# Kernel tuning notes

Measured on AMD Instinct MI355X. Metric: run time of the kernel, lower is better.

Reference implementation:

```python
import jax, jax.numpy as jnp
import numpy as np

B, T, D = 2, 2048, 1024
H, HD = 16, 64          # num_heads, head_dim (D == H*HD)
NM, DMIX, DDEC = 5, 32, 64  # 5 mix streams (r,k,v,w,g); LoRA ranks per source thresholds


def setup_inputs() -> dict:
    key = jax.random.key(0)
    ks = jax.random.split(key, 18)
    n = lambda i, shape, s: jax.random.normal(ks[i], shape, dtype=jnp.float32) * s
    return {
        "hidden_states": n(0, (B, T, D), 1.0),
        "time_maa_x": n(1, (1, 1, D), 0.5),
        "time_maa_r": n(2, (1, 1, D), 0.1),
        "time_maa_k": n(3, (1, 1, D), 0.1),
        "time_maa_v": n(4, (1, 1, D), 0.1),
        "time_maa_w": n(5, (1, 1, D), 0.1),
        "time_maa_g": n(6, (1, 1, D), 0.1),
        "time_maa_w1": n(7, (D, NM * DMIX), 0.01),
        "time_maa_w2": n(8, (NM, DMIX, D), 0.01),
        "time_decay": n(9, (1, 1, D), 0.5) - 2.0,  # decay_speed-like, negative mean
        "time_decay_w1": n(10, (D, DDEC), 0.01),
        "time_decay_w2": n(11, (DDEC, D), 0.01),
        "Wq": n(12, (D, D), 0.02),
        "Wk": n(13, (D, D), 0.02),
        "Wv": n(14, (D, D), 0.02),
        "Wo": n(15, (D, D), 0.02),
        "Wg": n(16, (D, D), 0.02),
        "bg": jnp.full((D,), 1.227, dtype=jnp.float32),  # gate bias init from source
    }


def _forward(hidden_states, time_maa_x, time_maa_r, time_maa_k, time_maa_v,
             time_maa_w, time_maa_g, time_maa_w1, time_maa_w2, time_decay,
             time_decay_w1, time_decay_w2, Wq, Wk, Wv, Wo, Wg, bg):
    x = hidden_states
    Bsz, Tlen, d = x.shape
    # token shift: dxprev = x_{t-1} - x_t (zeros at t=0)
    xprev = jnp.pad(x, ((0, 0), (1, 0), (0, 0)))[:, :Tlen]
    dxprev = xprev - x
    # data-dependent LoRA mixing producing 5 per-stream mix coefficients
    xxx = x + dxprev * time_maa_x
    mix = jnp.tanh(xxx @ time_maa_w1).reshape(Bsz, Tlen, NM, DMIX)
    mix = jnp.einsum('btfl,fld->fbtd', mix, time_maa_w2)  # (5, B, T, D)
    mr, mk, mv, mw, mg = mix
    xr = x + dxprev * (time_maa_r + mr)
    xk = x + dxprev * (time_maa_k + mk)
    xv = x + dxprev * (time_maa_v + mv)
    xw = x + dxprev * (time_maa_w + mw)
    xg = x + dxprev * (time_maa_g + mg)
    # projections -> (B, H, T, HD); num_kv_heads == num_heads so repeat_kv is identity
    q = (xr @ Wq).reshape(Bsz, Tlen, H, HD).transpose(0, 2, 1, 3)
    k = (xk @ Wk).reshape(Bsz, Tlen, H, HD).transpose(0, 2, 1, 3)
    v = (xv @ Wv).reshape(Bsz, Tlen, H, HD).transpose(0, 2, 1, 3)
    decay = time_decay + jnp.tanh(xw @ time_decay_w1) @ time_decay_w2
    g_log = -jnp.exp(decay.reshape(Bsz, Tlen, H, HD).transpose(0, 2, 1, 3))  # (B,H,T,HD), <= 0
    gate = jax.nn.silu(xg @ Wg + bg)
    # bonus term from source: k scaled by (1 - exp(g_log))
    k = k * (1.0 - jnp.exp(g_log))
    q = q * (HD ** -0.5)  # fla scale
    # gated linear attention: S_t = diag(exp(g_t)) S_{t-1} + k_t v_t^T ; o_t = q_t @ S_t
    def step(S, qkvg):
        qt, kt, vt, gt = qkvg                       # (B,H,HD) each
        S = S * jnp.exp(gt)[..., None] + kt[..., None] * vt[..., None, :]
        ot = jnp.einsum('bhk,bhkv->bhv', qt, S)
        return S, ot
    S0 = jnp.zeros((Bsz, H, HD, HD), dtype=jnp.float32)
    seq = (jnp.moveaxis(q, 2, 0), jnp.moveaxis(k, 2, 0),
           jnp.moveaxis(v, 2, 0), jnp.moveaxis(g_log, 2, 0))
    _, o = jax.lax.scan(step, S0, seq)              # (T, B, H, HD)
    o = jnp.moveaxis(o, 0, 1)                       # (B, T, H, HD)
    o = o.reshape(Bsz, Tlen, H * HD)
    return (o * gate) @ Wo


def reference(hidden_states, time_maa_x, time_maa_r, time_maa_k, time_maa_v,
              time_maa_w, time_maa_g, time_maa_w1, time_maa_w2, time_decay,
              time_decay_w1, time_decay_w2, Wq, Wk, Wv, Wo, Wg, bg):
    return _forward(hidden_states, time_maa_x, time_maa_r, time_maa_k, time_maa_v,
                    time_maa_w, time_maa_g, time_maa_w1, time_maa_w2, time_decay,
                    time_decay_w1, time_decay_w2, Wq, Wk, Wv, Wo, Wg, bg)
```

## Files before the change

kernel.cpp:

```cpp
#include <hip/hip_runtime.h>
#include <hip/hip_bf16.h>

typedef __hip_bfloat16 bf16;
typedef __bf16 bf16x8 __attribute__((ext_vector_type(8)));
typedef float f32x4 __attribute__((ext_vector_type(4)));

static constexpr size_t MB = 1ull << 20;

static constexpr size_t OFF_XXXQ = 0;
static constexpr size_t OFF_K    = 8  * MB;
static constexpr size_t OFF_V    = 16 * MB;
static constexpr size_t OFF_W    = 24 * MB;
static constexpr size_t OFF_GATE = 32 * MB;
static constexpr size_t OFF_WOT  = 40 * MB;
static constexpr size_t OFF_W1T  = 42 * MB;
static constexpr size_t OFF_WD1T = 42 * MB + 512 * 1024;
static constexpr size_t OFF_WD2T = 42 * MB + 768 * 1024;
static constexpr size_t OFF_MP   = 43 * MB;
static constexpr size_t OFF_DECT = 47 * MB;
static constexpr size_t OFF_XS   = 48 * MB;
static constexpr size_t OFF_WQT  = 56 * MB;
static constexpr size_t OFF_WKT  = 58 * MB;
static constexpr size_t OFF_WVT  = 60 * MB;
static constexpr size_t OFF_WGT  = 62 * MB;
static constexpr size_t OFF_SLOC = 43 * MB;
static constexpr size_t OFF_D    = 59 * MB;

__device__ __forceinline__ void async_ld16(const void* g, void* l) {
    __builtin_amdgcn_global_load_lds((const __attribute__((address_space(1))) void*)g,
                                     (__attribute__((address_space(3))) void*)l, 16, 0, 0);
}
__device__ __forceinline__ float bf2f(unsigned short u) {
    union { unsigned int i; float f; } x; x.i = ((unsigned int)u) << 16; return x.f;
}

__global__ void transpose_all(const float* __restrict__ Wq, const float* __restrict__ Wk,
                              const float* __restrict__ Wv, const float* __restrict__ Wg,
                              const float* __restrict__ Wo, const float* __restrict__ w1,
                              const float* __restrict__ dw1, const float* __restrict__ dw2,
                              bf16* __restrict__ wqt, bf16* __restrict__ wkt,
                              bf16* __restrict__ wvt, bf16* __restrict__ wgt,
                              bf16* __restrict__ wot, bf16* __restrict__ w1t,
                              bf16* __restrict__ wd1t, bf16* __restrict__ wd2t) {
    __shared__ bf16 tile[32][33];
    int id = blockIdx.x;
    const float* src; bf16* dst; int R, C, Cpad, local;
    if      (id < 1024) { src = Wq;  dst = wqt;  R = 1024; C = 1024; Cpad = 1024; local = id; }
    else if (id < 2048) { src = Wk;  dst = wkt;  R = 1024; C = 1024; Cpad = 1024; local = id - 1024; }
    else if (id < 3072) { src = Wv;  dst = wvt;  R = 1024; C = 1024; Cpad = 1024; local = id - 2048; }
    else if (id < 4096) { src = Wg;  dst = wgt;  R = 1024; C = 1024; Cpad = 1024; local = id - 3072; }
    else if (id < 5120) { src = Wo;  dst = wot;  R = 1024; C = 1024; Cpad = 1024; local = id - 4096; }
    else if (id < 5376) { src = w1;  dst = w1t;  R = 1024; C = 160;  Cpad = 256;  local = id - 5120; }
    else if (id < 5504) { src = dw1; dst = wd1t; R = 1024; C = 64;   Cpad = 128;  local = id - 5376; }
    else                { src = dw2; dst = wd2t; R = 64;   C = 1024; Cpad = 1024; local = id - 5504; }
    int Rb = R >> 5;
    int r0 = (local % Rb) * 32, c0 = (local / Rb) * 32;
    int tx = threadIdx.x, ty = threadIdx.y;
#pragma unroll
    for (int yy = 0; yy < 4; ++yy) {
        int r = r0 + ty + yy * 8, c = c0 + tx;
        float v = (r < R && c < C) ? src[(size_t)r * C + c] : 0.f;
        tile[ty + yy * 8][tx] = __float2bfloat16(v);
    }
    __syncthreads();
#pragma unroll
    for (int yy = 0; yy < 4; ++yy) {
        int c = c0 + ty + yy * 8, r = r0 + tx;
        if (c < Cpad && r < R) dst[(size_t)c * R + r] = tile[tx][ty + yy * 8];
    }
}

__global__ void prep_xxx(const float* __restrict__ x, const float* __restrict__ maa_x,
                         bf16* __restrict__ xxx) {
    int i = blockIdx.x * 256 + threadIdx.x;
    int d = i & 1023;
    int t = (i >> 10) & 2047;
    float xv = x[i];
    float xp = (t > 0) ? x[i - 1024] : 0.f;
    xxx[i] = __float2bfloat16(xv + (xp - xv) * maa_x[d]);
}

template<int EPI>
__global__ __launch_bounds__(256)
void gemm_bt(const bf16* __restrict__ A, int lda,
             const bf16* __restrict__ Bt, int ldb,
             void* __restrict__ Cout, int ldc,
             int K, const float* __restrict__ aux)
{
    __shared__ __align__(16) bf16 As[128 * 32];
    __shared__ __align__(16) bf16 Bs[128 * 32];
    const int m0 = blockIdx.x * 128;
    const int n0 = blockIdx.y * 128;
    const int tid = threadIdx.x;
    const int lane = tid & 63;
    const int w = tid >> 6;
    const int wm = w >> 1, wn = w & 1;
    const int row16 = lane & 15;
    const int quad = lane >> 4;

    f32x4 acc[4][4];
#pragma unroll
    for (int mi = 0; mi < 4; ++mi)
#pragma unroll
        for (int ni = 0; ni < 4; ++ni)
            acc[mi][ni] = (f32x4){0.f, 0.f, 0.f, 0.f};

    for (int k0 = 0; k0 < K; k0 += 32) {
        __syncthreads();
#pragma unroll
        for (int j = 0; j < 2; ++j) {
            int i = j * 256 + w * 64 + lane;
            int ri = i >> 2;
            int ci = (i & 3) * 8;
            const bf16* ga = A  + (size_t)(m0 + ri) * lda + (k0 + ci);
            const bf16* gb = Bt + (size_t)(n0 + ri) * ldb + (k0 + ci);
            bf16* la = As + (size_t)(j * 256 + w * 64) * 8;
            bf16* lb = Bs + (size_t)(j * 256 + w * 64) * 8;
            async_ld16(ga, la);
            async_ld16(gb, lb);
        }
        __syncthreads();
        bf16x8 af[4], bfr[4];
#pragma unroll
        for (int mi = 0; mi < 4; ++mi)
            af[mi] = *(const bf16x8*)(As + ((wm * 64 + mi * 16 + row16) * 32 + quad * 8));
#pragma unroll
        for (int ni = 0; ni < 4; ++ni)
            bfr[ni] = *(const bf16x8*)(Bs + ((wn * 64 + ni * 16 + row16) * 32 + quad * 8));
#pragma unroll
        for (int mi = 0; mi < 4; ++mi)
#pragma unroll
            for (int ni = 0; ni < 4; ++ni)
                acc[mi][ni] = __builtin_amdgcn_mfma_f32_16x16x32_bf16(af[mi], bfr[ni], acc[mi][ni], 0, 0, 0);
    }
#pragma unroll
    for (int mi = 0; mi < 4; ++mi)
#pragma unroll
        for (int ni = 0; ni < 4; ++ni)
#pragma unroll
            for (int r = 0; r < 4; ++r) {
                int gr = m0 + wm * 64 + mi * 16 + quad * 4 + r;
                int gc = n0 + wn * 64 + ni * 16 + row16;
                size_t ci = (size_t)gr * ldc + gc;
                float v = acc[mi][ni][r];
                if (EPI == 1) ((float*)Cout)[ci] = tanhf(v);
                else if (EPI == 2) ((bf16*)Cout)[ci] = __float2bfloat16(tanhf(v));
                else if (EPI == 3) {
                    float t = aux[gc] + v;
                    ((bf16*)Cout)[ci] = __float2bfloat16(expf(t));
                } else if (EPI == 4) {
                    float z = v + aux[gc];
                    ((bf16*)Cout)[ci] = __float2bfloat16(z / (1.f + expf(-z)));
                } else if (EPI == 5) {
                    ((bf16*)Cout)[ci] = __float2bfloat16(v);
                } else {
                    ((float*)Cout)[ci] = v;
                }
            }
}

__global__ __launch_bounds__(256)
void mix_stream(const float* __restrict__ mp,
                const float* __restrict__ w2,
                const float* __restrict__ x,
                const float* __restrict__ maa_f,
                int f,
                bf16* __restrict__ xs)
{
    __shared__ float mps[4][32];
    int dg = blockIdx.x;
    int r0 = blockIdx.y * 4;
    int tid = threadIdx.x;
    int d = dg * 256 + tid;
    if (tid < 128) {
        int rr = tid >> 5, l = tid & 31;
        mps[rr][l] = mp[(size_t)(r0 + rr) * 256 + f * 32 + l];
    }
    __syncthreads();
    float acc[4] = {0.f, 0.f, 0.f, 0.f};
#pragma unroll
    for (int l = 0; l < 32; ++l) {
        float wv = w2[(size_t)(f * 32 + l) * 1024 + d];
#pragma unroll
        for (int rr = 0; rr < 4; ++rr)
            acc[rr] = fmaf(mps[rr][l], wv, acc[rr]);
    }
    float mf = maa_f[d];
#pragma unroll
    for (int rr = 0; rr < 4; ++rr) {
        int r = r0 + rr;
        int t = r & 2047;
        size_t i = (size_t)r * 1024 + d;
        float xv = x[i];
        float xp = (t > 0) ? x[i - 1024] : 0.f;
        xs[i] = __float2bfloat16(xv + (xp - xv) * (mf + acc[rr]));
    }
}

__global__ __launch_bounds__(64)
void chunk_state(const bf16* __restrict__ k, const bf16* __restrict__ v,
                 const bf16* __restrict__ w,
                 float* __restrict__ Sloc, float* __restrict__ D)
{
    int c = blockIdx.x, bh = blockIdx.y;
    int b = bh >> 4, h = bh & 15;
    int lane = threadIdx.x;
    __shared__ __align__(16) float sh[2][64];
    size_t base = (size_t)b * 2048 * 1024 + (size_t)h * 64 + (size_t)c * 64 * 1024;

    float S[64];
#pragma unroll
    for (int i = 0; i < 64; ++i) S[i] = 0.f;
    float Dl = 1.f;

    const unsigned short* kp = (const unsigned short*)k;
    const unsigned short* vp = (const unsigned short*)v;
    const unsigned short* wp = (const unsigned short*)w;
    unsigned short kr[4], vr[4], wr[4];
#pragma unroll
    for (int j = 0; j < 4; ++j) {
        size_t a = base + (size_t)j * 1024 + lane;
        kr[j] = kp[a]; vr[j] = vp[a]; wr[j] = wp[a];
    }
    for (int t = 0; t < 64; ++t) {
        int slot = t & 3, p = t & 1;
        float kl = bf2f(kr[slot]);
        float vl = bf2f(vr[slot]);
        float wl = bf2f(wr[slot]);
        if (t + 4 < 64) {
            size_t a = base + (size_t)(t + 4) * 1024 + lane;
            kr[slot] = kp[a]; vr[slot] = vp[a]; wr[slot] = wp[a];
        }
        float el = __expf(-wl);
        float kb = kl * (1.f - el);
        Dl *= el;
        sh[p][lane] = vl;
        __syncthreads();
        const float4* v4 = (const float4*)sh[p];
#pragma unroll
        for (int vv = 0; vv < 16; ++vv) {
            float4 vx = v4[vv];
            int s = vv * 4;
            S[s + 0] = S[s + 0] * el + kb * vx.x;
            S[s + 1] = S[s + 1] * el + kb * vx.y;
            S[s + 2] = S[s + 2] * el + kb * vx.z;
            S[s + 3] = S[s + 3] * el + kb * vx.w;
        }
    }
    float* So = Sloc + ((size_t)bh * 32 + c) * 4096;
#pragma unroll
    for (int i = 0; i < 64; ++i) So[(size_t)i * 64 + lane] = S[i];
    D[((size_t)bh * 32 + c) * 64 + lane] = Dl;
}

__global__ __launch_bounds__(256)
void chunk_combine(float* __restrict__ Sloc, const float* __restrict__ D)
{
    int bh = blockIdx.x;
    int tid = threadIdx.x;
    int k = tid & 63, v0 = tid >> 6;
#pragma unroll
    for (int j = 0; j < 16; ++j) {
        int v = v0 + j * 4;
        float s = 0.f;
        for (int c = 0; c < 32; ++c) {
            size_t idx = ((size_t)bh * 32 + c) * 4096 + (size_t)v * 64 + k;
            float tmp = Sloc[idx];
            Sloc[idx] = s;
            s = s * D[((size_t)bh * 32 + c) * 64 + k] + tmp;
        }
    }
}

__global__ __launch_bounds__(64)
void chunk_out(const bf16* __restrict__ q, const bf16* __restrict__ k,
               const bf16* __restrict__ v, const bf16* __restrict__ w,
               const bf16* gate, const float* __restrict__ S0buf,
               bf16* ag)
{
    int c = blockIdx.x, bh = blockIdx.y;
    int b = bh >> 4, h = bh & 15;
    int lane = threadIdx.x;
    __shared__ __align__(16) float sh[2][3][64];
    size_t base = (size_t)b * 2048 * 1024 + (size_t)h * 64 + (size_t)c * 64 * 1024;

    float S[64];
    const float4* S0 = (const float4*)(S0buf + ((size_t)bh * 32 + c) * 4096 + (size_t)lane * 64);
#pragma unroll
    for (int i = 0; i < 16; ++i) {
        float4 x4 = S0[i];
        S[i * 4 + 0] = x4.x; S[i * 4 + 1] = x4.y; S[i * 4 + 2] = x4.z; S[i * 4 + 3] = x4.w;
    }

    const unsigned short* qp = (const unsigned short*)q;
    const unsigned short* kp = (const unsigned short*)k;
    const unsigned short* vp = (const unsigned short*)v;
    const unsigned short* wp = (const unsigned short*)w;
    const unsigned short* gp = (const unsigned short*)gate;
    unsigned short qr[4], kr[4], vr[4], wr[4], gr[4];
#pragma unroll
    for (int j = 0; j < 4; ++j) {
        size_t a = base + (size_t)j * 1024 + lane;
        qr[j] = qp[a]; kr[j] = kp[a]; vr[j] = vp[a]; wr[j] = wp[a]; gr[j] = gp[a];
    }
    for (int t = 0; t < 64; ++t) {
        int slot = t & 3, p = t & 1;
        float ql = bf2f(qr[slot]) * 0.125f;
        float kl = bf2f(kr[slot]);
        float vl = bf2f(vr[slot]);
        float wl = bf2f(wr[slot]);
        float gl = bf2f(gr[slot]);
        if (t + 4 < 64) {
            size_t a = base + (size_t)(t + 4) * 1024 + lane;
            qr[slot] = qp[a]; kr[slot] = kp[a]; vr[slot] = vp[a];
            wr[slot] = wp[a]; gr[slot] = gp[a];
        }
        float el = __expf(-wl);
        sh[p][0][lane] = ql;
        sh[p][1][lane] = kl * (1.f - el);
        sh[p][2][lane] = el;
        __syncthreads();
        const float4* q4 = (const float4*)sh[p][0];
        const float4* k4 = (const float4*)sh[p][1];
        const float4* e4 = (const float4*)sh[p][2];
        float a0 = 0.f, a1 = 0.f, a2 = 0.f, a3 = 0.f;
#pragma unroll
        for (int kk = 0; kk < 16; ++kk) {
            float4 qq = q4[kk], kx = k4[kk], ee = e4[kk];
            int s = kk * 4;
            S[s + 0] = S[s + 0] * ee.x + kx.x * vl; a0 += qq.x * S[s + 0];
            S[s + 1] = S[s + 1] * ee.y + kx.y * vl; a1 += qq.y * S[s + 1];
            S[s + 2] = S[s + 2] * ee.z + kx.z * vl; a2 += qq.z * S[s + 2];
            S[s + 3] = S[s + 3] * ee.w + kx.w * vl; a3 += qq.w * S[s + 3];
        }
        ag[base + (size_t)t * 1024 + lane] = __float2bfloat16(((a0 + a1) + (a2 + a3)) * gl);
    }
}

extern "C" void kernel_launch(void* const* d_in, const int* in_sizes, int n_in,
                              void* d_out, int out_size, void* d_ws, size_t ws_size,
                              hipStream_t stream) {
    const float* x    = (const float*)d_in[0];
    const float* maax = (const float*)d_in[1];
    const float* maar = (const float*)d_in[2];
    const float* maak = (const float*)d_in[3];
    const float* maav = (const float*)d_in[4];
    const float* maaw = (const float*)d_in[5];
    const float* maag = (const float*)d_in[6];
    const float* w1   = (const float*)d_in[7];
    const float* w2   = (const float*)d_in[8];
    const float* td   = (const float*)d_in[9];
    const float* dw1  = (const float*)d_in[10];
    const float* dw2  = (const float*)d_in[11];
    const float* Wq   = (const float*)d_in[12];
    const float* Wk   = (const float*)d_in[13];
    const float* Wv   = (const float*)d_in[14];
    const float* Wo   = (const float*)d_in[15];
    const float* Wg   = (const float*)d_in[16];
    const float* bg   = (const float*)d_in[17];

    char* ws = (char*)d_ws;
    bf16*  xxx   = (bf16*) (ws + OFF_XXXQ);
    bf16*  qb    = (bf16*) (ws + OFF_XXXQ);
    bf16*  kb    = (bf16*) (ws + OFF_K);
    bf16*  vb    = (bf16*) (ws + OFF_V);
    bf16*  wb    = (bf16*) (ws + OFF_W);
    bf16*  gateb = (bf16*) (ws + OFF_GATE);
    bf16*  wot   = (bf16*) (ws + OFF_WOT);
    bf16*  w1t   = (bf16*) (ws + OFF_W1T);
    bf16*  wd1t  = (bf16*) (ws + OFF_WD1T);
    bf16*  wd2t  = (bf16*) (ws + OFF_WD2T);
    float* mp    = (float*)(ws + OFF_MP);
    bf16*  dect  = (bf16*) (ws + OFF_DECT);
    bf16*  xs    = (bf16*) (ws + OFF_XS);
    bf16*  wqt   = (bf16*) (ws + OFF_WQT);
    bf16*  wkt   = (bf16*) (ws + OFF_WKT);
    bf16*  wvt   = (bf16*) (ws + OFF_WVT);
    bf16*  wgt   = (bf16*) (ws + OFF_WGT);
    float* Sloc  = (float*)(ws + OFF_SLOC);
    float* Dbuf  = (float*)(ws + OFF_D);

    transpose_all<<<5568, dim3(32, 8), 0, stream>>>(Wq, Wk, Wv, Wg, Wo, w1, dw1, dw2,
                                                    wqt, wkt, wvt, wgt, wot, w1t, wd1t, wd2t);

    prep_xxx<<<16384, 256, 0, stream>>>(x, maax, xxx);

    gemm_bt<1><<<dim3(32, 2), 256, 0, stream>>>(xxx, 1024, w1t, 1024, mp, 256, 1024, nullptr);

    mix_stream<<<dim3(4, 1024), 256, 0, stream>>>(mp, w2, x, maaw, 3, xs);
    gemm_bt<2><<<dim3(32, 1), 256, 0, stream>>>(xs, 1024, wd1t, 1024, dect, 128, 1024, nullptr);
    gemm_bt<3><<<dim3(32, 8), 256, 0, stream>>>(dect, 128, wd2t, 64, wb, 1024, 64, td);

    mix_stream<<<dim3(4, 1024), 256, 0, stream>>>(mp, w2, x, maar, 0, xs);
    gemm_bt<5><<<dim3(32, 8), 256, 0, stream>>>(xs, 1024, wqt, 1024, qb, 1024, 1024, nullptr);

    mix_stream<<<dim3(4, 1024), 256, 0, stream>>>(mp, w2, x, maak, 1, xs);
    gemm_bt<5><<<dim3(32, 8), 256, 0, stream>>>(xs, 1024, wkt, 1024, kb, 1024, 1024, nullptr);

    mix_stream<<<dim3(4, 1024), 256, 0, stream>>>(mp, w2, x, maav, 2, xs);
    gemm_bt<5><<<dim3(32, 8), 256, 0, stream>>>(xs, 1024, wvt, 1024, vb, 1024, 1024, nullptr);

    mix_stream<<<dim3(4, 1024), 256, 0, stream>>>(mp, w2, x, maag, 4, xs);
    gemm_bt<4><<<dim3(32, 8), 256, 0, stream>>>(xs, 1024, wgt, 1024, gateb, 1024, 1024, bg);

    chunk_state  <<<dim3(32, 32),  64, 0, stream>>>(kb, vb, wb, Sloc, Dbuf);
    chunk_combine<<<32,           256, 0, stream>>>(Sloc, Dbuf);
    chunk_out    <<<dim3(32, 32),  64, 0, stream>>>(qb, kb, vb, wb, gateb, Sloc, gateb);

    gemm_bt<6><<<dim3(32, 8), 256, 0, stream>>>(gateb, 1024, wot, 1024, (float*)d_out, 1024, 1024, nullptr);

    (void)in_sizes; (void)n_in; (void)out_size; (void)ws_size;
}
```

Measured before the change: 567.2 us.

## Batch mix/projection pairs, halve scan chunk length, store chunk states in fp16

Mix-stream and projection GEMM launches are paired: one kernel builds two mixed inputs, and a z-indexed GEMM computes two projections per launch, which gives fuller grids and fewer launches. The chunked scan now uses 32-token chunks (64 chunks per head) to double block parallelism and shorten each block's serial loop. Chunk states are stored in fp16, and the combine kernel keeps 16 running sums in registers to cut memory traffic. The fp16 state storage risks precision loss, and the longer serial combine loop adds latency.

```diff
diff --git a/kernel.cpp b/kernel.cpp
--- a/kernel.cpp
+++ b/kernel.cpp
@@ -4,27 +4,30 @@
 typedef __hip_bfloat16 bf16;
 typedef __bf16 bf16x8 __attribute__((ext_vector_type(8)));
 typedef float f32x4 __attribute__((ext_vector_type(4)));
+typedef _Float16 h8 __attribute__((ext_vector_type(8)));
 
 static constexpr size_t MB = 1ull << 20;
+static constexpr size_t KB = 1024;
 
 static constexpr size_t OFF_XXXQ = 0;
-static constexpr size_t OFF_K    = 8  * MB;
+static constexpr size_t OFF_K    = 8 * MB;
 static constexpr size_t OFF_V    = 16 * MB;
 static constexpr size_t OFF_W    = 24 * MB;
+static constexpr size_t OFF_WQT  = 32 * MB;
+static constexpr size_t OFF_WKT  = 34 * MB;
+static constexpr size_t OFF_MP   = 36 * MB;
 static constexpr size_t OFF_GATE = 32 * MB;
-static constexpr size_t OFF_WOT  = 40 * MB;
-static constexpr size_t OFF_W1T  = 42 * MB;
-static constexpr size_t OFF_WD1T = 42 * MB + 512 * 1024;
-static constexpr size_t OFF_WD2T = 42 * MB + 768 * 1024;
-static constexpr size_t OFF_MP   = 43 * MB;
-static constexpr size_t OFF_DECT = 47 * MB;
-static constexpr size_t OFF_XS   = 48 * MB;
-static constexpr size_t OFF_WQT  = 56 * MB;
-static constexpr size_t OFF_WKT  = 58 * MB;
-static constexpr size_t OFF_WVT  = 60 * MB;
-static constexpr size_t OFF_WGT  = 62 * MB;
-static constexpr size_t OFF_SLOC = 43 * MB;
-static constexpr size_t OFF_D    = 59 * MB;
+static constexpr size_t OFF_XS0  = 40 * MB;
+static constexpr size_t OFF_XS1  = 48 * MB;
+static constexpr size_t OFF_SLOC = 40 * MB;
+static constexpr size_t OFF_WVT  = 56 * MB;
+static constexpr size_t OFF_WGT  = 58 * MB;
+static constexpr size_t OFF_WOT  = 60 * MB;
+static constexpr size_t OFF_W1T  = 62 * MB;
+static constexpr size_t OFF_D    = 62 * MB;
+static constexpr size_t OFF_WD1T = 62 * MB + 512 * KB;
+static constexpr size_t OFF_WD2T = 62 * MB + 768 * KB;
+static constexpr size_t OFF_DECT = 63 * MB;
 
 __device__ __forceinline__ void async_ld16(const void* g, void* l) {
     __builtin_amdgcn_global_load_lds((const __attribute__((address_space(1))) void*)g,
@@ -112,12 +115,8 @@
             int i = j * 256 + w * 64 + lane;
             int ri = i >> 2;
             int ci = (i & 3) * 8;
-            const bf16* ga = A  + (size_t)(m0 + ri) * lda + (k0 + ci);
-            const bf16* gb = Bt + (size_t)(n0 + ri) * ldb + (k0 + ci);
-            bf16* la = As + (size_t)(j * 256 + w * 64) * 8;
-            bf16* lb = Bs + (size_t)(j * 256 + w * 64) * 8;
-            async_ld16(ga, la);
-            async_ld16(gb, lb);
+            async_ld16(A  + (size_t)(m0 + ri) * lda + (k0 + ci), As + (size_t)(j * 256 + w * 64) * 8);
+            async_ld16(Bt + (size_t)(n0 + ri) * ldb + (k0 + ci), Bs + (size_t)(j * 256 + w * 64) * 8);
         }
         __syncthreads();
         bf16x8 af[4], bfr[4];
@@ -148,29 +147,90 @@
                 else if (EPI == 3) {
                     float t = aux[gc] + v;
                     ((bf16*)Cout)[ci] = __float2bfloat16(expf(t));
-                } else if (EPI == 4) {
-                    float z = v + aux[gc];
-                    ((bf16*)Cout)[ci] = __float2bfloat16(z / (1.f + expf(-z)));
-                } else if (EPI == 5) {
-                    ((bf16*)Cout)[ci] = __float2bfloat16(v);
                 } else {
                     ((float*)Cout)[ci] = v;
                 }
             }
 }
 
+template<int EPI1>
 __global__ __launch_bounds__(256)
-void mix_stream(const float* __restrict__ mp,
-                const float* __restrict__ w2,
-                const float* __restrict__ x,
-                const float* __restrict__ maa_f,
-                int f,
-                bf16* __restrict__ xs)
+void gemm_bt2(const bf16* __restrict__ A0, const bf16* __restrict__ A1, int lda,
+              const bf16* __restrict__ B0, const bf16* __restrict__ B1, int ldb,
+              bf16* __restrict__ C0, bf16* __restrict__ C1, int ldc,
+              int K, const float* __restrict__ aux)
+{
+    __shared__ __align__(16) bf16 As[128 * 32];
+    __shared__ __align__(16) bf16 Bs[128 * 32];
+    const int z = blockIdx.z;
+    const bf16* A  = z ? A1 : A0;
+    const bf16* Bt = z ? B1 : B0;
+    bf16* Cout     = z ? C1 : C0;
+    const int m0 = blockIdx.x * 128;
+    const int n0 = blockIdx.y * 128;
+    const int tid = threadIdx.x;
+    const int lane = tid & 63;
+    const int w = tid >> 6;
+    const int wm = w >> 1, wn = w & 1;
+    const int row16 = lane & 15;
+    const int quad = lane >> 4;
+
+    f32x4 acc[4][4];
+#pragma unroll
+    for (int mi = 0; mi < 4; ++mi)
+#pragma unroll
+        for (int ni = 0; ni < 4; ++ni)
+            acc[mi][ni] = (f32x4){0.f, 0.f, 0.f, 0.f};
+
+    for (int k0 = 0; k0 < K; k0 += 32) {
+        __syncthreads();
+#pragma unroll
+        for (int j = 0; j < 2; ++j) {
+            int i = j * 256 + w * 64 + lane;
+            int ri = i >> 2;
+            int ci = (i & 3) * 8;
+            async_ld16(A  + (size_t)(m0 + ri) * lda + (k0 + ci), As + (size_t)(j * 256 + w * 64) * 8);
+            async_ld16(Bt + (size_t)(n0 + ri) * ldb + (k0 + ci), Bs + (size_t)(j * 256 + w * 64) * 8);
+        }
+        __syncthreads();
+        bf16x8 af[4], bfr[4];
+#pragma unroll
+        for (int mi = 0; mi < 4; ++mi)
+            af[mi] = *(const bf16x8*)(As + ((wm * 64 + mi * 16 + row16) * 32 + quad * 8));
+#pragma unroll
+        for (int ni = 0; ni < 4; ++ni)
+            bfr[ni] = *(const bf16x8*)(Bs + ((wn * 64 + ni * 16 + row16) * 32 + quad * 8));
+#pragma unroll
+        for (int mi = 0; mi < 4; ++mi)
+#pragma unroll
+            for (int ni = 0; ni < 4; ++ni)
+                acc[mi][ni] = __builtin_amdgcn_mfma_f32_16x16x32_bf16(af[mi], bfr[ni], acc[mi][ni], 0, 0, 0);
+    }
+#pragma unroll
+    for (int mi = 0; mi < 4; ++mi)
+#pragma unroll
+        for (int ni = 0; ni < 4; ++ni)
+#pragma unroll
+            for (int r = 0; r < 4; ++r) {
+                int gr = m0 + wm * 64 + mi * 16 + quad * 4 + r;
+                int gc = n0 + wn * 64 + ni * 16 + row16;
+                size_t ci = (size_t)gr * ldc + gc;
+                float v = acc[mi][ni][r];
+                if (z == 0 || EPI1 == 5) Cout[ci] = __float2bfloat16(v);
+                else {
+                    float zz = v + aux[gc];
+                    Cout[ci] = __float2bfloat16(zz / (1.f + expf(-zz)));
+                }
+            }
+}
+
+__global__ __launch_bounds__(256)
+void mix_stream(const float* __restrict__ mp, const float* __restrict__ w2,
+                const float* __restrict__ x, const float* __restrict__ maa_f,
+                int f, bf16* __restrict__ xs)
 {
     __shared__ float mps[4][32];
-    int dg = blockIdx.x;
-    int r0 = blockIdx.y * 4;
-    int tid = threadIdx.x;
+    int dg = blockIdx.x, r0 = blockIdx.y * 4, tid = threadIdx.x;
     int d = dg * 256 + tid;
     if (tid < 128) {
         int rr = tid >> 5, l = tid & 31;
@@ -182,14 +242,12 @@
     for (int l = 0; l < 32; ++l) {
         float wv = w2[(size_t)(f * 32 + l) * 1024 + d];
 #pragma unroll
-        for (int rr = 0; rr < 4; ++rr)
-            acc[rr] = fmaf(mps[rr][l], wv, acc[rr]);
+        for (int rr = 0; rr < 4; ++rr) acc[rr] = fmaf(mps[rr][l], wv, acc[rr]);
     }
     float mf = maa_f[d];
 #pragma unroll
     for (int rr = 0; rr < 4; ++rr) {
-        int r = r0 + rr;
-        int t = r & 2047;
+        int r = r0 + rr, t = r & 2047;
         size_t i = (size_t)r * 1024 + d;
         float xv = x[i];
         float xp = (t > 0) ? x[i - 1024] : 0.f;
@@ -197,16 +255,55 @@
     }
 }
 
+__global__ __launch_bounds__(256)
+void mix_stream2(const float* __restrict__ mp, const float* __restrict__ w2,
+                 const float* __restrict__ x,
+                 const float* __restrict__ maa_a, const float* __restrict__ maa_b,
+                 int fa, int fb, bf16* __restrict__ xsa, bf16* __restrict__ xsb)
+{
+    __shared__ float mpsa[4][32], mpsb[4][32];
+    int dg = blockIdx.x, r0 = blockIdx.y * 4, tid = threadIdx.x;
+    int d = dg * 256 + tid;
+    if (tid < 128) {
+        int rr = tid >> 5, l = tid & 31;
+        mpsa[rr][l] = mp[(size_t)(r0 + rr) * 256 + fa * 32 + l];
+        mpsb[rr][l] = mp[(size_t)(r0 + rr) * 256 + fb * 32 + l];
+    }
+    __syncthreads();
+    float acca[4] = {0.f, 0.f, 0.f, 0.f}, accb[4] = {0.f, 0.f, 0.f, 0.f};
+#pragma unroll
+    for (int l = 0; l < 32; ++l) {
+        float wa = w2[(size_t)(fa * 32 + l) * 1024 + d];
+        float wbv = w2[(size_t)(fb * 32 + l) * 1024 + d];
+#pragma unroll
+        for (int rr = 0; rr < 4; ++rr) {
+            acca[rr] = fmaf(mpsa[rr][l], wa, acca[rr]);
+            accb[rr] = fmaf(mpsb[rr][l], wbv, accb[rr]);
+        }
+    }
+    float ma = maa_a[d], mb = maa_b[d];
+#pragma unroll
+    for (int rr = 0; rr < 4; ++rr) {
+        int r = r0 + rr, t = r & 2047;
+        size_t i = (size_t)r * 1024 + d;
+        float xv = x[i];
+        float xp = (t > 0) ? x[i - 1024] : 0.f;
+        float dx = xp - xv;
+        xsa[i] = __float2bfloat16(xv + dx * (ma + acca[rr]));
+        xsb[i] = __float2bfloat16(xv + dx * (mb + accb[rr]));
+    }
+}
+
 __global__ __launch_bounds__(64)
 void chunk_state(const bf16* __restrict__ k, const bf16* __restrict__ v,
                  const bf16* __restrict__ w,
-                 float* __restrict__ Sloc, float* __restrict__ D)
+                 _Float16* __restrict__ Sloc, float* __restrict__ D)
 {
     int c = blockIdx.x, bh = blockIdx.y;
     int b = bh >> 4, h = bh & 15;
     int lane = threadIdx.x;
     __shared__ __align__(16) float sh[2][64];
-    size_t base = (size_t)b * 2048 * 1024 + (size_t)h * 64 + (size_t)c * 64 * 1024;
+    size_t base = (size_t)b * 2048 * 1024 + (size_t)h * 64 + (size_t)c * 32 * 1024;
 
     float S[64];
 #pragma unroll
@@ -222,12 +319,12 @@
         size_t a = base + (size_t)j * 1024 + lane;
         kr[j] = kp[a]; vr[j] = vp[a]; wr[j] = wp[a];
     }
-    for (int t = 0; t < 64; ++t) {
+    for (int t = 0; t < 32; ++t) {
         int slot = t & 3, p = t & 1;
         float kl = bf2f(kr[slot]);
         float vl = bf2f(vr[slot]);
         float wl = bf2f(wr[slot]);
-        if (t + 4 < 64) {
+        if (t + 4 < 32) {
             size_t a = base + (size_t)(t + 4) * 1024 + lane;
             kr[slot] = kp[a]; vr[slot] = vp[a]; wr[slot] = wp[a];
         }
@@ -247,27 +344,30 @@
             S[s + 3] = S[s + 3] * el + kb * vx.w;
         }
     }
-    float* So = Sloc + ((size_t)bh * 32 + c) * 4096;
-#pragma unroll
-    for (int i = 0; i < 64; ++i) So[(size_t)i * 64 + lane] = S[i];
-    D[((size_t)bh * 32 + c) * 64 + lane] = Dl;
+    _Float16* So = Sloc + ((size_t)bh * 64 + c) * 4096;
+#pragma unroll
+    for (int i = 0; i < 64; ++i) So[(size_t)i * 64 + lane] = (_Float16)S[i];
+    D[((size_t)bh * 64 + c) * 64 + lane] = Dl;
 }
 
 __global__ __launch_bounds__(256)
-void chunk_combine(float* __restrict__ Sloc, const float* __restrict__ D)
+void chunk_combine(_Float16* __restrict__ Sloc, const float* __restrict__ D)
 {
     int bh = blockIdx.x;
     int tid = threadIdx.x;
     int k = tid & 63, v0 = tid >> 6;
-#pragma unroll
-    for (int j = 0; j < 16; ++j) {
-        int v = v0 + j * 4;
-        float s = 0.f;
-        for (int c = 0; c < 32; ++c) {
-            size_t idx = ((size_t)bh * 32 + c) * 4096 + (size_t)v * 64 + k;
-            float tmp = Sloc[idx];
-            Sloc[idx] = s;
-            s = s * D[((size_t)bh * 32 + c) * 64 + k] + tmp;
+    float s[16];
+#pragma unroll
+    for (int j = 0; j < 16; ++j) s[j] = 0.f;
+    for (int c = 0; c < 64; ++c) {
+        float Dk = D[((size_t)bh * 64 + c) * 64 + k];
+        size_t basei = ((size_t)bh * 64 + c) * 4096 + k;
+#pragma unroll
+        for (int j = 0; j < 16; ++j) {
+            size_t idx = basei + (size_t)(v0 + j * 4) * 64;
+            float tmp = (float)Sloc[idx];
+            Sloc[idx] = (_Float16)s[j];
+            s[j] = s[j] * Dk + tmp;
         }
     }
 }
@@ -275,21 +375,22 @@
 __global__ __launch_bounds__(64)
 void chunk_out(const bf16* __restrict__ q, const bf16* __restrict__ k,
                const bf16* __restrict__ v, const bf16* __restrict__ w,
-               const bf16* gate, const float* __restrict__ S0buf,
+               const bf16* gate, const _Float16* __restrict__ S0buf,
                bf16* ag)
 {
     int c = blockIdx.x, bh = blockIdx.y;
     int b = bh >> 4, h = bh & 15;
     int lane = threadIdx.x;
     __shared__ __align__(16) float sh[2][3][64];
-    size_t base = (size_t)b * 2048 * 1024 + (size_t)h * 64 + (size_t)c * 64 * 1024;
+    size_t base = (size_t)b * 2048 * 1024 + (size_t)h * 64 + (size_t)c * 32 * 1024;
 
     float S[64];
-    const float4* S0 = (const float4*)(S0buf + ((size_t)bh * 32 + c) * 4096 + (size_t)lane * 64);
-#pragma unroll
-    for (int i = 0; i < 16; ++i) {
-        float4 x4 = S0[i];
-        S[i * 4 + 0] = x4.x; S[i * 4 + 1] = x4.y; S[i * 4 + 2] = x4.z; S[i * 4 + 3] = x4.w;
+    const h8* S0 = (const h8*)(S0buf + ((size_t)bh * 64 + c) * 4096 + (size_t)lane * 64);
+#pragma unroll
+    for (int i = 0; i < 8; ++i) {
+        h8 hv = S0[i];
+#pragma unroll
+        for (int j = 0; j < 8; ++j) S[i * 8 + j] = (float)hv[j];
     }
 
     const unsigned short* qp = (const unsigned short*)q;
@@ -303,14 +404,14 @@
         size_t a = base + (size_t)j * 1024 + lane;
         qr[j] = qp[a]; kr[j] = kp[a]; vr[j] = vp[a]; wr[j] = wp[a]; gr[j] = gp[a];
     }
-    for (int t = 0; t < 64; ++t) {
+    for (int t = 0; t < 32; ++t) {
         int slot = t & 3, p = t & 1;
         float ql = bf2f(qr[slot]) * 0.125f;
         float kl = bf2f(kr[slot]);
         float vl = bf2f(vr[slot]);
         float wl = bf2f(wr[slot]);
         float gl = bf2f(gr[slot]);
-        if (t + 4 < 64) {
+        if (t + 4 < 32) {
             size_t a = base + (size_t)(t + 4) * 1024 + lane;
             qr[slot] = qp[a]; kr[slot] = kp[a]; vr[slot] = vp[a];
             wr[slot] = wp[a]; gr[slot] = gp[a];
@@ -366,46 +467,42 @@
     bf16*  vb    = (bf16*) (ws + OFF_V);
     bf16*  wb    = (bf16*) (ws + OFF_W);
     bf16*  gateb = (bf16*) (ws + OFF_GATE);
+    bf16*  wqt   = (bf16*) (ws + OFF_WQT);
+    bf16*  wkt   = (bf16*) (ws + OFF_WKT);
+    float* mp    = (float*)(ws + OFF_MP);
+    bf16*  xs0   = (bf16*) (ws + OFF_XS0);
+    bf16*  xs1   = (bf16*) (ws + OFF_XS1);
+    bf16*  wvt   = (bf16*) (ws + OFF_WVT);
+    bf16*  wgt   = (bf16*) (ws + OFF_WGT);
     bf16*  wot   = (bf16*) (ws + OFF_WOT);
     bf16*  w1t   = (bf16*) (ws + OFF_W1T);
     bf16*  wd1t  = (bf16*) (ws + OFF_WD1T);
     bf16*  wd2t  = (bf16*) (ws + OFF_WD2T);
-    float* mp    = (float*)(ws + OFF_MP);
     bf16*  dect  = (bf16*) (ws + OFF_DECT);
-    bf16*  xs    = (bf16*) (ws + OFF_XS);
-    bf16*  wqt   = (bf16*) (ws + OFF_WQT);
-    bf16*  wkt   = (bf16*) (ws + OFF_WKT);
-    bf16*  wvt   = (bf16*) (ws + OFF_WVT);
-    bf16*  wgt   = (bf16*) (ws + OFF_WGT);
-    float* Sloc  = (float*)(ws + OFF_SLOC);
+    _Float16* Sloc = (_Float16*)(ws + OFF_SLOC);
     float* Dbuf  = (float*)(ws + OFF_D);
 
     transpose_all<<<5568, dim3(32, 8), 0, stream>>>(Wq, Wk, Wv, Wg, Wo, w1, dw1, dw2,
                                                     wqt, wkt, wvt, wgt, wot, w1t, wd1t, wd2t);
-
     prep_xxx<<<16384, 256, 0, stream>>>(x, maax, xxx);
 
     gemm_bt<1><<<dim3(32, 2), 256, 0, stream>>>(xxx, 1024, w1t, 1024, mp, 256, 1024, nullptr);
 
-    mix_stream<<<dim3(4, 1024), 256, 0, stream>>>(mp, w2, x, maaw, 3, xs);
-    gemm_bt<2><<<dim3(32, 1), 256, 0, stream>>>(xs, 1024, wd1t, 1024, dect, 128, 1024, nullptr);
+    mix_stream<<<dim3(4, 1024), 256, 0, stream>>>(mp, w2, x, maaw, 3, xs0);
+    gemm_bt<2><<<dim3(32, 1), 256, 0, stream>>>(xs0, 1024, wd1t, 1024, dect, 128, 1024, nullptr);
     gemm_bt<3><<<dim3(32, 8), 256, 0, stream>>>(dect, 128, wd2t, 64, wb, 1024, 64, td);
 
-    mix_stream<<<dim3(4, 1024), 256, 0, stream>>>(mp, w2, x, maar, 0, xs);
-    gemm_bt<5><<<dim3(32, 8), 256, 0, stream>>>(xs, 1024, wqt, 1024, qb, 1024, 1024, nullptr);
-
-    mix_stream<<<dim3(4, 1024), 256, 0, stream>>>(mp, w2, x, maak, 1, xs);
-    gemm_bt<5><<<dim3(32, 8), 256, 0, stream>>>(xs, 1024, wkt, 1024, kb, 1024, 1024, nullptr);
-
-    mix_stream<<<dim3(4, 1024), 256, 0, stream>>>(mp, w2, x, maav, 2, xs);
-    gemm_bt<5><<<dim3(32, 8), 256, 0, stream>>>(xs, 1024, wvt, 1024, vb, 1024, 1024, nullptr);
-
-    mix_stream<<<dim3(4, 1024), 256, 0, stream>>>(mp, w2, x, maag, 4, xs);
-    gemm_bt<4><<<dim3(32, 8), 256, 0, stream>>>(xs, 1024, wgt, 1024, gateb, 1024, 1024, bg);
-
-    chunk_state  <<<dim3(32, 32),  64, 0, stream>>>(kb, vb, wb, Sloc, Dbuf);
+    mix_stream2<<<dim3(4, 1024), 256, 0, stream>>>(mp, w2, x, maar, maak, 0, 1, xs0, xs1);
+    gemm_bt2<5><<<dim3(32, 8, 2), 256, 0, stream>>>(xs0, xs1, 1024, wqt, wkt, 1024,
+                                                    qb, kb, 1024, 1024, nullptr);
+
+    mix_stream2<<<dim3(4, 1024), 256, 0, stream>>>(mp, w2, x, maav, maag, 2, 4, xs0, xs1);
+    gemm_bt2<4><<<dim3(32, 8, 2), 256, 0, stream>>>(xs0, xs1, 1024, wvt, wgt, 1024,
+                                                    vb, gateb, 1024, 1024, bg);
+
+    chunk_state  <<<dim3(64, 32),  64, 0, stream>>>(kb, vb, wb, Sloc, Dbuf);
     chunk_combine<<<32,           256, 0, stream>>>(Sloc, Dbuf);
-    chunk_out    <<<dim3(32, 32),  64, 0, stream>>>(qb, kb, vb, wb, gateb, Sloc, gateb);
+    chunk_out    <<<dim3(64, 32),  64, 0, stream>>>(qb, kb, vb, wb, gateb, Sloc, gateb);
 
     gemm_bt<6><<<dim3(32, 8), 256, 0, stream>>>(gateb, 1024, wot, 1024, (float*)d_out, 1024, 1024, nullptr);
 
```

Result: faster. 502.2 us (-11.5%).
